# Kernel tuning notes

Hardware: AMD Instinct MI355X
Metric: run time of the kernel (lower is better)

Reference implementation:

```python
import jax, jax.numpy as jnp
import numpy as np

HIDDEN = 2048
INPUT = 128
BATCH = 2048


def setup_inputs() -> dict:
    key = jax.random.key(0)
    k = jax.random.split(key, 7)
    inp = {
        "input": jax.random.normal(k[0], (BATCH, INPUT), dtype=jnp.float32),
        "hx_real": jax.random.normal(k[1], (BATCH, HIDDEN), dtype=jnp.float32),
        "hx_imag": jax.random.normal(k[2], (BATCH, HIDDEN), dtype=jnp.float32),
        "W_unitary": jax.random.normal(k[3], (5 * HIDDEN, INPUT), dtype=jnp.float32) / np.sqrt(INPUT),
        "b_unitary": jax.random.normal(k[4], (5 * HIDDEN,), dtype=jnp.float32) * 0.01,
        "beta": jnp.zeros((HIDDEN,), dtype=jnp.float32),
        "permutation": jax.random.permutation(k[5], HIDDEN).astype(jnp.int32),
    }
    return inp


def _householder_apply(v, h):
    # (I - 2 v v^H) h = h - 2 v (v^H h); same math as materializing the matrix.
    proj = jnp.sum(jnp.conj(v) * h, axis=-1, keepdims=True)
    return h - 2.0 * v * proj


def reference(input, hx_real, hx_imag, W_unitary, b_unitary, beta, permutation):
    hx = hx_real + 1j * hx_imag  # (B, H) complex64
    up = input @ W_unitary.T + b_unitary  # (B, 5H)
    phases = jnp.exp(1j * up)  # complex64, unit modulus
    d1, d2, d3, r1, r2 = jnp.split(phases, 5, axis=-1)

    h = jnp.fft.fft(d1 * hx, axis=-1)
    h = _householder_apply(r1, h)
    h = jnp.fft.ifft(d2 * h[:, permutation], axis=-1)
    h = d3 * _householder_apply(r2, h)

    # ModReLU: relu(|z| + beta) * exp(1j * angle(z))
    mag = jnp.abs(h)
    new_mag = jax.nn.relu(mag + beta)
    h = new_mag * jnp.exp(1j * jnp.angle(h))
    return h
```

## Files before the change

kernel.cpp:

```cpp
#include <hip/hip_runtime.h>
#include <hip/hip_fp16.h>

#define HID 2048
#define FIVEH 10240
#define INP 128
#define BATCH 2048

typedef _Float16 half8 __attribute__((ext_vector_type(8)));
typedef float f32x4 __attribute__((ext_vector_type(4)));

__device__ __forceinline__ half8 cvt8(const float* p) {
  float4 a = *(const float4*)p;
  float4 b = *(const float4*)(p + 4);
  half8 h;
  h[0] = (_Float16)a.x; h[1] = (_Float16)a.y; h[2] = (_Float16)a.z; h[3] = (_Float16)a.w;
  h[4] = (_Float16)b.x; h[5] = (_Float16)b.y; h[6] = (_Float16)b.z; h[7] = (_Float16)b.w;
  return h;
}

#define WSTRIDE 136
__global__ __launch_bounds__(256) void gemm_up(const float* __restrict__ A,
                                               const float* __restrict__ W,
                                               const float* __restrict__ bias,
                                               _Float16* __restrict__ up16,
                                               int row0, int nrows) {
  __shared__ _Float16 Ws[128 * WSTRIDE];
  int tid = threadIdx.x, wave = tid >> 6, lane = tid & 63;
  int bx = blockIdx.x;
  int by = blockIdx.y;
  int nl = lane & 15, quad = lane >> 4;

  {
    const float* src = W + (size_t)(bx * 128) * INP;
#pragma unroll
    for (int it = 0; it < 8; ++it) {
      int n = (it * 256 + tid) * 8;
      int col = n >> 7, k = n & 127;
      *(half8*)(Ws + col * WSTRIDE + k) = cvt8(src + n);
    }
  }

  half8 af[2][4];
  int rowbase = row0 + by * 128 + wave * 32;
#pragma unroll
  for (int mt = 0; mt < 2; ++mt) {
    const float* ar = A + (size_t)(rowbase + mt * 16 + nl) * INP + quad * 8;
#pragma unroll
    for (int ks = 0; ks < 4; ++ks) af[mt][ks] = cvt8(ar + ks * 32);
  }
  __syncthreads();

  f32x4 acc[2][8];
#pragma unroll
  for (int nt = 0; nt < 8; ++nt) {
    half8 bf[4];
#pragma unroll
    for (int ks = 0; ks < 4; ++ks)
      bf[ks] = *(const half8*)(Ws + (nt * 16 + nl) * WSTRIDE + quad * 8 + ks * 32);
#pragma unroll
    for (int mt = 0; mt < 2; ++mt) {
      f32x4 a = {0.f, 0.f, 0.f, 0.f};
#pragma unroll
      for (int ks = 0; ks < 4; ++ks)
        a = __builtin_amdgcn_mfma_f32_16x16x32_f16(af[mt][ks], bf[ks], a, 0, 0, 0);
      acc[mt][nt] = a;
    }
  }
  __syncthreads();

#pragma unroll
  for (int nt = 0; nt < 8; ++nt) {
    float bv = bias[bx * 128 + nt * 16 + nl];
#pragma unroll
    for (int mt = 0; mt < 2; ++mt) {
      int rl = wave * 32 + mt * 16 + quad * 4;
#pragma unroll
      for (int r = 0; r < 4; ++r)
        Ws[(rl + r) * WSTRIDE + nt * 16 + nl] = (_Float16)(acc[mt][nt][r] + bv);
    }
  }
  __syncthreads();

#pragma unroll
  for (int it = 0; it < 8; ++it) {
    int v = it * 256 + tid;
    int r = v >> 4, c8 = (v & 15) * 8;
    *(half8*)(up16 + (size_t)(by * 128 + r) * FIVEH + bx * 128 + c8) =
        *(const half8*)(Ws + r * WSTRIDE + c8);
  }
}

__device__ __forceinline__ float2 h2ld(const __half2* p, int i) {
  return __half22float2(p[i]);
}
__device__ __forceinline__ void h2st(__half2* p, int i, float x, float y) {
  p[i] = __floats2half2_rn(x, y);
}

__device__ __forceinline__ void fft_r4(__half2*& src, __half2*& dst, int tid, float sgn) {
#pragma unroll
  for (int t = 0; t < 4; ++t) {
    int i = tid + (t << 8);
    float2 a = h2ld(src, i), b = h2ld(src, i + 1024);
    h2st(dst, 2 * i,     a.x + b.x, a.y + b.y);
    h2st(dst, 2 * i + 1, a.x - b.x, a.y - b.y);
  }
  __syncthreads();
  { __half2* t = src; src = dst; dst = t; }

#pragma unroll
  for (int pass = 0; pass < 5; ++pass) {
    const int L = 2 << (2 * pass);
    const float co = sgn * 1.5707963267948966f / (float)L;
#pragma unroll
    for (int t = 0; t < 2; ++t) {
      int i = tid + (t << 8);
      int k = i & (L - 1);
      int base4 = ((i - k) << 2) + k;
      float2 x0 = h2ld(src, i),        x1 = h2ld(src, i + 512);
      float2 x2 = h2ld(src, i + 1024), x3 = h2ld(src, i + 1536);
      float ang = co * (float)k;
      float s1, c1; __sincosf(ang, &s1, &c1);
      float c2 = c1 * c1 - s1 * s1, s2 = 2.f * c1 * s1;
      float c3 = c1 * c2 - s1 * s2, s3 = c1 * s2 + s1 * c2;
      float y1r = x1.x * c1 - x1.y * s1, y1i = x1.x * s1 + x1.y * c1;
      float y2r = x2.x * c2 - x2.y * s2, y2i = x2.x * s2 + x2.y * c2;
      float y3r = x3.x * c3 - x3.y * s3, y3i = x3.x * s3 + x3.y * c3;
      float t0r = x0.x + y2r, t0i = x0.y + y2i;
      float t1r = x0.x - y2r, t1i = x0.y - y2i;
      float t2r = y1r + y3r, t2i = y1i + y3i;
      float t3r = y1r - y3r, t3i = y1i - y3i;
      h2st(dst, base4,         t0r + t2r, t0i + t2i);
      h2st(dst, base4 + 2 * L, t0r - t2r, t0i - t2i);
      h2st(dst, base4 + L,     t1r - sgn * t3i, t1i + sgn * t3r);
      h2st(dst, base4 + 3 * L, t1r + sgn * t3i, t1i - sgn * t3r);
    }
    __syncthreads();
    { __half2* t = src; src = dst; dst = t; }
  }
}

__device__ __forceinline__ void block_reduce2(float& pr, float& pi,
                                              float* redr, float* redi, int tid) {
  for (int off = 32; off > 0; off >>= 1) {
    pr += __shfl_down(pr, off, 64);
    pi += __shfl_down(pi, off, 64);
  }
  if ((tid & 63) == 0) { redr[tid >> 6] = pr; redi[tid >> 6] = pi; }
  __syncthreads();
  pr = redr[0] + redr[1] + redr[2] + redr[3];
  pi = redi[0] + redi[1] + redi[2] + redi[3];
  __syncthreads();
}

#define ROW_PIPELINE(UP)                                                        \
  __half2 *ca = sA, *cb = sB;                                                   \
  fft_r4(ca, cb, tid, -1.0f);                                                   \
  float cc[8], ss[8];                                                           \
  {                                                                             \
    float pr = 0.f, pi = 0.f;                                                   \
    _Pragma("unroll") for (int e = 0; e < 8; ++e) {                             \
      int k = tid + (e << 8);                                                   \
      float sv, cv; __sincosf(UP(e, 3), &sv, &cv);                              \
      cc[e] = cv; ss[e] = sv;                                                   \
      float2 h = h2ld(ca, k);                                                   \
      pr += cv * h.x + sv * h.y;                                                \
      pi += cv * h.y - sv * h.x;                                                \
    }                                                                           \
    block_reduce2(pr, pi, redr, redi, tid);                                     \
    _Pragma("unroll") for (int e = 0; e < 8; ++e) {                             \
      int k = tid + (e << 8);                                                   \
      float2 h = h2ld(ca, k);                                                   \
      h2st(ca, k, h.x - 2.f * (cc[e] * pr - ss[e] * pi),                        \
                  h.y - 2.f * (cc[e] * pi + ss[e] * pr));                       \
    }                                                                           \
  }                                                                             \
  __syncthreads();                                                              \
  const float invN = 1.0f / (float)HID;                                         \
  _Pragma("unroll") for (int e = 0; e < 8; ++e) {                               \
    int k = tid + (e << 8);                                                     \
    float sv, cv; __sincosf(UP(e, 1), &sv, &cv);                                \
    float2 h = h2ld(ca, perm[k]);                                               \
    h2st(cb, k, (cv * h.x - sv * h.y) * invN, (cv * h.y + sv * h.x) * invN);    \
  }                                                                             \
  __syncthreads();                                                              \
  { __half2* t = ca; ca = cb; cb = t; }                                         \
  fft_r4(ca, cb, tid, 1.0f);                                                    \
  float prj_r, prj_i;                                                           \
  {                                                                             \
    float pr = 0.f, pi = 0.f;                                                   \
    _Pragma("unroll") for (int e = 0; e < 8; ++e) {                             \
      int k = tid + (e << 8);                                                   \
      float sv, cv; __sincosf(UP(e, 4), &sv, &cv);                              \
      cc[e] = cv; ss[e] = sv;                                                   \
      float2 h = h2ld(ca, k);                                                   \
      pr += cv * h.x + sv * h.y;                                                \
      pi += cv * h.y - sv * h.x;                                                \
    }                                                                           \
    block_reduce2(pr, pi, redr, redi, tid);                                     \
    prj_r = pr; prj_i = pi;                                                     \
  }                                                                             \
  _Pragma("unroll") for (int e = 0; e < 8; ++e) {                               \
    int k = tid + (e << 8);                                                     \
    float2 h = h2ld(ca, k);                                                     \
    float hr = h.x - 2.f * (cc[e] * prj_r - ss[e] * prj_i);                     \
    float hi = h.y - 2.f * (cc[e] * prj_i + ss[e] * prj_r);                     \
    float s3, c3; __sincosf(UP(e, 2), &s3, &c3);                                \
    float zr = c3 * hr - s3 * hi;                                               \
    float zi = c3 * hi + s3 * hr;                                               \
    float mag = sqrtf(zr * zr + zi * zi);                                       \
    float nm = mag + beta[k];                                                   \
    nm = nm > 0.f ? nm : 0.f;                                                   \
    float orr, oii;                                                             \
    if (mag > 0.f) { float sc = nm / mag; orr = zr * sc; oii = zi * sc; }       \
    else { orr = nm; oii = 0.f; }                                               \
    long m = (long)b * HID + k;                                                 \
    if (omode == 1) {                                                           \
      const long half = (long)BATCH * HID;                                      \
      if (half + m < out_size_l) { out[m] = orr; out[half + m] = oii; }         \
    } else if (omode == 0) {                                                    \
      if (2 * m + 1 < out_size_l) {                                             \
        float2 o; o.x = orr; o.y = oii;                                         \
        *(float2*)(out + 2 * m) = o;                                            \
      }                                                                         \
    } else {                                                                    \
      if (m < out_size_l) out[m] = orr;                                         \
    }                                                                           \
  }

__global__ __launch_bounds__(256, 8) void urnn_row(const _Float16* __restrict__ up16,
                                                   const float* __restrict__ hxr,
                                                   const float* __restrict__ hxi,
                                                   const float* __restrict__ beta,
                                                   const int* __restrict__ perm,
                                                   float* __restrict__ out,
                                                   int row0, long out_size_l, int omode) {
  __shared__ __half2 sA[HID], sB[HID];
  __shared__ float redr[4], redi[4];

  int tid = threadIdx.x;
  int b = row0 + blockIdx.x;
  const _Float16* uprow = up16 + (size_t)blockIdx.x * FIVEH;
#define UPG(e, s) ((float)uprow[(s) * HID + tid + ((e) << 8)])

#pragma unroll
  for (int e = 0; e < 8; ++e) {
    int k = tid + (e << 8);
    float sv, cv; __sincosf(UPG(e, 0), &sv, &cv);
    float hr = hxr[(size_t)b * HID + k];
    float hi = hxi[(size_t)b * HID + k];
    h2st(sA, k, cv * hr - sv * hi, cv * hi + sv * hr);
  }
  __syncthreads();
  ROW_PIPELINE(UPG)
#undef UPG
}

__global__ __launch_bounds__(256) void urnn_fused(const float* __restrict__ A,
                                                  const float* __restrict__ W,
                                                  const float* __restrict__ bias,
                                                  const float* __restrict__ hxr,
                                                  const float* __restrict__ hxi,
                                                  const float* __restrict__ beta,
                                                  const int* __restrict__ perm,
                                                  float* __restrict__ out,
                                                  long out_size_l, int omode) {
  __shared__ __half2 sA[HID], sB[HID];
  __shared__ float redr[4], redi[4];
  __shared__ float4 xs4[INP / 4];

  int tid = threadIdx.x;
  int b = blockIdx.x;

  if (tid < INP / 4) xs4[tid] = ((const float4*)(A + (size_t)b * INP))[tid];
  __syncthreads();

  float upreg[40];
#pragma unroll
  for (int se = 0; se < 40; ++se) {
    int n = ((se >> 3) << 11) + ((se & 7) << 8) + tid;
    upreg[se] = bias[n];
  }
  for (int kb = 0; kb < 4; ++kb) {
    float4 xv[8];
#pragma unroll
    for (int j = 0; j < 8; ++j) xv[j] = xs4[kb * 8 + j];
#pragma unroll
    for (int se = 0; se < 40; ++se) {
      int n = ((se >> 3) << 11) + ((se & 7) << 8) + tid;
      const float4* wr = (const float4*)(W + (size_t)n * INP + (kb << 5));
      float a = 0.f;
#pragma unroll
      for (int j = 0; j < 8; ++j) {
        float4 wv = wr[j];
        a += xv[j].x * wv.x + xv[j].y * wv.y + xv[j].z * wv.z + xv[j].w * wv.w;
      }
      upreg[se] += a;
    }
  }
#define UPR(e, s) (upreg[(s) * 8 + (e)])
#pragma unroll
  for (int e = 0; e < 8; ++e) {
    int k = tid + (e << 8);
    float sv, cv; __sincosf(UPR(e, 0), &sv, &cv);
    float hr = hxr[(size_t)b * HID + k];
    float hi = hxi[(size_t)b * HID + k];
    h2st(sA, k, cv * hr - sv * hi, cv * hi + sv * hr);
  }
  __syncthreads();
  ROW_PIPELINE(UPR)
#undef UPR
}

extern "C" void kernel_launch(void* const* d_in, const int* in_sizes, int n_in,
                              void* d_out, int out_size, void* d_ws, size_t ws_size,
                              hipStream_t stream) {
  const float* input   = (const float*)d_in[0];
  const float* hx_real = (const float*)d_in[1];
  const float* hx_imag = (const float*)d_in[2];
  const float* W       = (const float*)d_in[3];
  const float* bvec    = (const float*)d_in[4];
  const float* beta    = (const float*)d_in[5];
  const int*   perm    = (const int*)d_in[6];

  int omode;
  if (out_size == BATCH * HID) omode = 2;
  else if (out_size == 2 * BATCH * HID) omode = 1;
  else omode = 0;

  const size_t rowbytes = (size_t)FIVEH * sizeof(_Float16);
  long chunk = (long)(ws_size / rowbytes);
  if (chunk > BATCH) chunk = BATCH;
  chunk &= ~127L;

  if (chunk >= 128) {
    _Float16* up16 = (_Float16*)d_ws;
    for (long row0 = 0; row0 < BATCH; row0 += chunk) {
      int rows = (int)((row0 + chunk <= BATCH) ? chunk : (BATCH - row0));
      dim3 g(FIVEH / 128, rows / 128);
      gemm_up<<<g, 256, 0, stream>>>(input, W, bvec, up16, (int)row0, rows);
      urnn_row<<<rows, 256, 0, stream>>>(up16, hx_real, hx_imag, beta, perm,
                                         (float*)d_out, (int)row0, (long)out_size, omode);
    }
  } else {
    urnn_fused<<<BATCH, 256, 0, stream>>>(input, W, bvec, hx_real, hx_imag, beta, perm,
                                          (float*)d_out, (long)out_size, omode);
  }
}
```

Before: 155.4 us.

## Fuse FFT first stages in registers and keep last stage outputs in registers

Restructures the 2048-point FFT as a register radix-8 head, three templated radix-4 LDS passes, and a radix-4 tail that writes into registers, instead of a radix-2 pass plus five radix-4 passes through shared memory. The phase-multiply input and the permuted/d2 input go straight into the head stage, and the Householder reductions read FFT outputs from registers. Twiddles in the middle passes are hoisted out of the per-element loop through compile-time L. This removes two LDS round trips and two barriers per FFT, at the cost of more register pressure and a different element-to-thread mapping, which must stay consistent with the Householder and ModReLU indexing.

```diff
diff --git a/kernel.cpp b/kernel.cpp
--- a/kernel.cpp
+++ b/kernel.cpp
@@ -97,46 +97,92 @@
   p[i] = __floats2half2_rn(x, y);
 }
 
-__device__ __forceinline__ void fft_r4(__half2*& src, __half2*& dst, int tid, float sgn) {
-#pragma unroll
-  for (int t = 0; t < 4; ++t) {
+__device__ __forceinline__ void fft_head(const float2 v[8], __half2* dst, int tid, float sgn) {
+  const float R2 = 0.70710678118654752f;
+  float2 o[8];
+  {
+    float x0r = v[0].x + v[4].x, x0i = v[0].y + v[4].y;
+    float x1r = v[1].x + v[5].x, x1i = v[1].y + v[5].y;
+    float x2r = v[2].x + v[6].x, x2i = v[2].y + v[6].y;
+    float x3r = v[3].x + v[7].x, x3i = v[3].y + v[7].y;
+    float t0r = x0r + x2r, t0i = x0i + x2i, t1r = x0r - x2r, t1i = x0i - x2i;
+    float t2r = x1r + x3r, t2i = x1i + x3i, t3r = x1r - x3r, t3i = x1i - x3i;
+    o[0].x = t0r + t2r;       o[0].y = t0i + t2i;
+    o[4].x = t0r - t2r;       o[4].y = t0i - t2i;
+    o[2].x = t1r - sgn * t3i; o[2].y = t1i + sgn * t3r;
+    o[6].x = t1r + sgn * t3i; o[6].y = t1i - sgn * t3r;
+  }
+  {
+    float x0r = v[0].x - v[4].x, x0i = v[0].y - v[4].y;
+    float x1r = v[1].x - v[5].x, x1i = v[1].y - v[5].y;
+    float x2r = v[2].x - v[6].x, x2i = v[2].y - v[6].y;
+    float x3r = v[3].x - v[7].x, x3i = v[3].y - v[7].y;
+    float y1r = (x1r - sgn * x1i) * R2,  y1i = (sgn * x1r + x1i) * R2;
+    float y2r = -sgn * x2i,              y2i = sgn * x2r;
+    float y3r = -(x3r + sgn * x3i) * R2, y3i = (sgn * x3r - x3i) * R2;
+    float t0r = x0r + y2r, t0i = x0i + y2i, t1r = x0r - y2r, t1i = x0i - y2i;
+    float t2r = y1r + y3r, t2i = y1i + y3i, t3r = y1r - y3r, t3i = y1i - y3i;
+    o[1].x = t0r + t2r;       o[1].y = t0i + t2i;
+    o[5].x = t0r - t2r;       o[5].y = t0i - t2i;
+    o[3].x = t1r - sgn * t3i; o[3].y = t1i + sgn * t3r;
+    o[7].x = t1r + sgn * t3i; o[7].y = t1i - sgn * t3r;
+  }
+  __half2* base = dst + 8 * tid;
+#pragma unroll
+  for (int j = 0; j < 8; ++j) h2st(base, j, o[j].x, o[j].y);
+}
+
+template <int L>
+__device__ __forceinline__ void fft_mid(const __half2* __restrict__ src,
+                                        __half2* __restrict__ dst, int tid, float sgn) {
+  static_assert(256 % L == 0, "twiddle hoist requires 256 % L == 0");
+  const int k = tid & (L - 1);
+  float s1, c1;
+  __sincosf(sgn * (1.5707963267948966f / (float)L) * (float)k, &s1, &c1);
+  float c2 = c1 * c1 - s1 * s1, s2 = 2.f * c1 * s1;
+  float c3 = c1 * c2 - s1 * s2, s3 = c1 * s2 + s1 * c2;
+#pragma unroll
+  for (int t = 0; t < 2; ++t) {
     int i = tid + (t << 8);
-    float2 a = h2ld(src, i), b = h2ld(src, i + 1024);
-    h2st(dst, 2 * i,     a.x + b.x, a.y + b.y);
-    h2st(dst, 2 * i + 1, a.x - b.x, a.y - b.y);
-  }
-  __syncthreads();
-  { __half2* t = src; src = dst; dst = t; }
-
-#pragma unroll
-  for (int pass = 0; pass < 5; ++pass) {
-    const int L = 2 << (2 * pass);
-    const float co = sgn * 1.5707963267948966f / (float)L;
-#pragma unroll
-    for (int t = 0; t < 2; ++t) {
-      int i = tid + (t << 8);
-      int k = i & (L - 1);
-      int base4 = ((i - k) << 2) + k;
-      float2 x0 = h2ld(src, i),        x1 = h2ld(src, i + 512);
-      float2 x2 = h2ld(src, i + 1024), x3 = h2ld(src, i + 1536);
-      float ang = co * (float)k;
-      float s1, c1; __sincosf(ang, &s1, &c1);
-      float c2 = c1 * c1 - s1 * s1, s2 = 2.f * c1 * s1;
-      float c3 = c1 * c2 - s1 * s2, s3 = c1 * s2 + s1 * c2;
-      float y1r = x1.x * c1 - x1.y * s1, y1i = x1.x * s1 + x1.y * c1;
-      float y2r = x2.x * c2 - x2.y * s2, y2i = x2.x * s2 + x2.y * c2;
-      float y3r = x3.x * c3 - x3.y * s3, y3i = x3.x * s3 + x3.y * c3;
-      float t0r = x0.x + y2r, t0i = x0.y + y2i;
-      float t1r = x0.x - y2r, t1i = x0.y - y2i;
-      float t2r = y1r + y3r, t2i = y1i + y3i;
-      float t3r = y1r - y3r, t3i = y1i - y3i;
-      h2st(dst, base4,         t0r + t2r, t0i + t2i);
-      h2st(dst, base4 + 2 * L, t0r - t2r, t0i - t2i);
-      h2st(dst, base4 + L,     t1r - sgn * t3i, t1i + sgn * t3r);
-      h2st(dst, base4 + 3 * L, t1r + sgn * t3i, t1i - sgn * t3r);
-    }
-    __syncthreads();
-    { __half2* t = src; src = dst; dst = t; }
+    int base4 = ((i - k) << 2) + k;
+    float2 x0 = h2ld(src, i),        x1 = h2ld(src, i + 512);
+    float2 x2 = h2ld(src, i + 1024), x3 = h2ld(src, i + 1536);
+    float y1r = x1.x * c1 - x1.y * s1, y1i = x1.x * s1 + x1.y * c1;
+    float y2r = x2.x * c2 - x2.y * s2, y2i = x2.x * s2 + x2.y * c2;
+    float y3r = x3.x * c3 - x3.y * s3, y3i = x3.x * s3 + x3.y * c3;
+    float t0r = x0.x + y2r, t0i = x0.y + y2i;
+    float t1r = x0.x - y2r, t1i = x0.y - y2i;
+    float t2r = y1r + y3r, t2i = y1i + y3i;
+    float t3r = y1r - y3r, t3i = y1i - y3i;
+    h2st(dst, base4,         t0r + t2r, t0i + t2i);
+    h2st(dst, base4 + 2 * L, t0r - t2r, t0i - t2i);
+    h2st(dst, base4 + L,     t1r - sgn * t3i, t1i + sgn * t3r);
+    h2st(dst, base4 + 3 * L, t1r + sgn * t3i, t1i - sgn * t3r);
+  }
+}
+
+__device__ __forceinline__ void fft_tail(const __half2* __restrict__ src, float2 h[8],
+                                         int tid, float sgn) {
+#pragma unroll
+  for (int t = 0; t < 2; ++t) {
+    int i = tid + (t << 8);
+    float s1, c1;
+    __sincosf(sgn * (1.5707963267948966f / 512.f) * (float)i, &s1, &c1);
+    float c2 = c1 * c1 - s1 * s1, s2 = 2.f * c1 * s1;
+    float c3 = c1 * c2 - s1 * s2, s3 = c1 * s2 + s1 * c2;
+    float2 x0 = h2ld(src, i),        x1 = h2ld(src, i + 512);
+    float2 x2 = h2ld(src, i + 1024), x3 = h2ld(src, i + 1536);
+    float y1r = x1.x * c1 - x1.y * s1, y1i = x1.x * s1 + x1.y * c1;
+    float y2r = x2.x * c2 - x2.y * s2, y2i = x2.x * s2 + x2.y * c2;
+    float y3r = x3.x * c3 - x3.y * s3, y3i = x3.x * s3 + x3.y * c3;
+    float t0r = x0.x + y2r, t0i = x0.y + y2i;
+    float t1r = x0.x - y2r, t1i = x0.y - y2i;
+    float t2r = y1r + y3r, t2i = y1i + y3i;
+    float t3r = y1r - y3r, t3i = y1i - y3i;
+    h[t].x     = t0r + t2r;       h[t].y     = t0i + t2i;
+    h[t + 4].x = t0r - t2r;       h[t + 4].y = t0i - t2i;
+    h[t + 2].x = t1r - sgn * t3i; h[t + 2].y = t1i + sgn * t3r;
+    h[t + 6].x = t1r + sgn * t3i; h[t + 6].y = t1i - sgn * t3r;
   }
 }
 
@@ -154,57 +200,73 @@
 }
 
 #define ROW_PIPELINE(UP)                                                        \
-  __half2 *ca = sA, *cb = sB;                                                   \
-  fft_r4(ca, cb, tid, -1.0f);                                                   \
+  float2 hreg[8];                                                               \
+  {                                                                             \
+    float2 v[8];                                                                \
+    _Pragma("unroll") for (int e = 0; e < 8; ++e) {                             \
+      int k = tid + (e << 8);                                                   \
+      float sv, cv; __sincosf(UP(e, 0), &sv, &cv);                              \
+      float hr = hxr[(size_t)b * HID + k];                                      \
+      float hi = hxi[(size_t)b * HID + k];                                      \
+      v[e].x = cv * hr - sv * hi; v[e].y = cv * hi + sv * hr;                   \
+    }                                                                           \
+    fft_head(v, sA, tid, -1.f);                                                 \
+  }                                                                             \
+  __syncthreads();                                                              \
+  fft_mid<8>(sA, sB, tid, -1.f);   __syncthreads();                             \
+  fft_mid<32>(sB, sA, tid, -1.f);  __syncthreads();                             \
+  fft_mid<128>(sA, sB, tid, -1.f); __syncthreads();                             \
+  fft_tail(sB, hreg, tid, -1.f);                                                \
   float cc[8], ss[8];                                                           \
   {                                                                             \
     float pr = 0.f, pi = 0.f;                                                   \
     _Pragma("unroll") for (int e = 0; e < 8; ++e) {                             \
-      int k = tid + (e << 8);                                                   \
       float sv, cv; __sincosf(UP(e, 3), &sv, &cv);                              \
       cc[e] = cv; ss[e] = sv;                                                   \
-      float2 h = h2ld(ca, k);                                                   \
-      pr += cv * h.x + sv * h.y;                                                \
-      pi += cv * h.y - sv * h.x;                                                \
+      pr += cv * hreg[e].x + sv * hreg[e].y;                                    \
+      pi += cv * hreg[e].y - sv * hreg[e].x;                                    \
     }                                                                           \
     block_reduce2(pr, pi, redr, redi, tid);                                     \
     _Pragma("unroll") for (int e = 0; e < 8; ++e) {                             \
       int k = tid + (e << 8);                                                   \
-      float2 h = h2ld(ca, k);                                                   \
-      h2st(ca, k, h.x - 2.f * (cc[e] * pr - ss[e] * pi),                        \
-                  h.y - 2.f * (cc[e] * pi + ss[e] * pr));                       \
+      h2st(sA, k, hreg[e].x - 2.f * (cc[e] * pr - ss[e] * pi),                  \
+                  hreg[e].y - 2.f * (cc[e] * pi + ss[e] * pr));                 \
     }                                                                           \
   }                                                                             \
   __syncthreads();                                                              \
-  const float invN = 1.0f / (float)HID;                                         \
-  _Pragma("unroll") for (int e = 0; e < 8; ++e) {                               \
-    int k = tid + (e << 8);                                                     \
-    float sv, cv; __sincosf(UP(e, 1), &sv, &cv);                                \
-    float2 h = h2ld(ca, perm[k]);                                               \
-    h2st(cb, k, (cv * h.x - sv * h.y) * invN, (cv * h.y + sv * h.x) * invN);    \
+  {                                                                             \
+    const float invN = 1.0f / (float)HID;                                       \
+    float2 v[8];                                                                \
+    _Pragma("unroll") for (int e = 0; e < 8; ++e) {                             \
+      int k = tid + (e << 8);                                                   \
+      float sv, cv; __sincosf(UP(e, 1), &sv, &cv);                              \
+      float2 hh = h2ld(sA, perm[k]);                                            \
+      v[e].x = (cv * hh.x - sv * hh.y) * invN;                                  \
+      v[e].y = (cv * hh.y + sv * hh.x) * invN;                                  \
+    }                                                                           \
+    fft_head(v, sB, tid, 1.f);                                                  \
   }                                                                             \
   __syncthreads();                                                              \
-  { __half2* t = ca; ca = cb; cb = t; }                                         \
-  fft_r4(ca, cb, tid, 1.0f);                                                    \
+  fft_mid<8>(sB, sA, tid, 1.f);   __syncthreads();                              \
+  fft_mid<32>(sA, sB, tid, 1.f);  __syncthreads();                              \
+  fft_mid<128>(sB, sA, tid, 1.f); __syncthreads();                              \
+  fft_tail(sA, hreg, tid, 1.f);                                                 \
   float prj_r, prj_i;                                                           \
   {                                                                             \
     float pr = 0.f, pi = 0.f;                                                   \
     _Pragma("unroll") for (int e = 0; e < 8; ++e) {                             \
-      int k = tid + (e << 8);                                                   \
       float sv, cv; __sincosf(UP(e, 4), &sv, &cv);                              \
       cc[e] = cv; ss[e] = sv;                                                   \
-      float2 h = h2ld(ca, k);                                                   \
-      pr += cv * h.x + sv * h.y;                                                \
-      pi += cv * h.y - sv * h.x;                                                \
+      pr += cv * hreg[e].x + sv * hreg[e].y;                                    \
+      pi += cv * hreg[e].y - sv * hreg[e].x;                                    \
     }                                                                           \
     block_reduce2(pr, pi, redr, redi, tid);                                     \
     prj_r = pr; prj_i = pi;                                                     \
   }                                                                             \
   _Pragma("unroll") for (int e = 0; e < 8; ++e) {                               \
     int k = tid + (e << 8);                                                     \
-    float2 h = h2ld(ca, k);                                                     \
-    float hr = h.x - 2.f * (cc[e] * prj_r - ss[e] * prj_i);                     \
-    float hi = h.y - 2.f * (cc[e] * prj_i + ss[e] * prj_r);                     \
+    float hr = hreg[e].x - 2.f * (cc[e] * prj_r - ss[e] * prj_i);               \
+    float hi = hreg[e].y - 2.f * (cc[e] * prj_i + ss[e] * prj_r);               \
     float s3, c3; __sincosf(UP(e, 2), &s3, &c3);                                \
     float zr = c3 * hr - s3 * hi;                                               \
     float zi = c3 * hi + s3 * hr;                                               \
@@ -242,16 +304,6 @@
   int b = row0 + blockIdx.x;
   const _Float16* uprow = up16 + (size_t)blockIdx.x * FIVEH;
 #define UPG(e, s) ((float)uprow[(s) * HID + tid + ((e) << 8)])
-
-#pragma unroll
-  for (int e = 0; e < 8; ++e) {
-    int k = tid + (e << 8);
-    float sv, cv; __sincosf(UPG(e, 0), &sv, &cv);
-    float hr = hxr[(size_t)b * HID + k];
-    float hi = hxi[(size_t)b * HID + k];
-    h2st(sA, k, cv * hr - sv * hi, cv * hi + sv * hr);
-  }
-  __syncthreads();
   ROW_PIPELINE(UPG)
 #undef UPG
 }
@@ -299,15 +351,6 @@
     }
   }
 #define UPR(e, s) (upreg[(s) * 8 + (e)])
-#pragma unroll
-  for (int e = 0; e < 8; ++e) {
-    int k = tid + (e << 8);
-    float sv, cv; __sincosf(UPR(e, 0), &sv, &cv);
-    float hr = hxr[(size_t)b * HID + k];
-    float hi = hxi[(size_t)b * HID + k];
-    h2st(sA, k, cv * hr - sv * hi, cv * hi + sv * hr);
-  }
-  __syncthreads();
   ROW_PIPELINE(UPR)
 #undef UPR
 }
```

Result: faster. 151.1 us (-2.8%).
